# Performance work log

Hardware: AMD Instinct MI355X
Metric: run time of the kernel (lower is better)

## Reference

```python
import jax, jax.numpy as jnp
import numpy as np
import math

POOL = 7          # RoIAlign output_size
SR = 2            # sampling_ratio


def _roi_align(feat, boxes, bidx):
    """torchvision RoIAlign, aligned=False, spatial_scale=1.0, sampling_ratio=2.
    feat: [B,C,H,W]; boxes: [N,4] (x1,y1,x2,y2) in pixel coords of this level;
    bidx: [N] int batch indices. Returns [N,C,POOL,POOL]."""
    B, C, H, W = feat.shape
    x1, y1, x2, y2 = boxes[:, 0], boxes[:, 1], boxes[:, 2], boxes[:, 3]
    roi_w = jnp.maximum(x2 - x1, 1.0)
    roi_h = jnp.maximum(y2 - y1, 1.0)
    bin_w = roi_w / POOL
    bin_h = roi_h / POOL
    # sample-point offsets within the ROI, in bin units: [POOL, SR]
    off = jnp.arange(POOL, dtype=feat.dtype)[:, None] + (jnp.arange(SR, dtype=feat.dtype)[None, :] + 0.5) / SR
    ys = y1[:, None, None] + bin_h[:, None, None] * off  # [N,POOL,SR]
    xs = x1[:, None, None] + bin_w[:, None, None] * off  # [N,POOL,SR]

    def prep(c, size):
        valid = (c > -1.0) & (c < size)
        c = jnp.clip(c, 0.0, size - 1)
        lo = jnp.floor(c).astype(jnp.int32)
        hi = jnp.minimum(lo + 1, size - 1)
        return lo, hi, c - lo, valid

    y_lo, y_hi, fy, vy = prep(ys, H)
    x_lo, x_hi, fx, vx = prep(xs, W)

    b = bidx.astype(jnp.int32)[:, None, None, None, None]  # [N,1,1,1,1]

    def gather(yi, xi):
        # -> [N,POOL,SR,POOL,SR,C] (advanced indices broadcast, channel slice last)
        return feat[b, :, yi[:, :, :, None, None], xi[:, None, None, :, :]]

    hy = (1.0 - fy)[:, :, :, None, None, None]
    ly = fy[:, :, :, None, None, None]
    hx = (1.0 - fx)[:, None, None, :, :, None]
    lx = fx[:, None, None, :, :, None]
    v = (gather(y_lo, x_lo) * hy * hx + gather(y_lo, x_hi) * hy * lx
         + gather(y_hi, x_lo) * ly * hx + gather(y_hi, x_hi) * ly * lx)
    valid = (vy[:, :, :, None, None] & vx[:, None, None, :, :])[..., None]
    v = jnp.where(valid, v, 0.0)
    out = v.mean(axis=(2, 4))          # average over SRxSR samples -> [N,POOL,POOL,C]
    return out.transpose(0, 3, 1, 2)   # [N,C,POOL,POOL]


def setup_inputs() -> dict:
    key = jax.random.key(0)
    k2, k3, k4, k5, kxy, kwh, kbi = jax.random.split(key, 7)
    N = 1000
    p2 = jax.random.normal(k2, (2, 256, 256, 256), dtype=jnp.float32)
    p3 = jax.random.normal(k3, (2, 256, 128, 128), dtype=jnp.float32)
    p4 = jax.random.normal(k4, (2, 256, 64, 64), dtype=jnp.float32)
    p5 = jax.random.normal(k5, (2, 256, 32, 32), dtype=jnp.float32)
    xy = jax.random.uniform(kxy, (N, 2), minval=0.0, maxval=0.7)
    wh = jax.random.uniform(kwh, (N, 2), minval=0.02, maxval=0.3)
    rpn_bbox = jnp.concatenate([xy, xy + wh], axis=1)  # (x1,y1,x2,y2) normalized
    box_index = jax.random.randint(kbi, (N,), 0, 2, dtype=jnp.int32)
    return {"p2": p2, "p3": p3, "p4": p4, "p5": p5,
            "rpn_bbox": rpn_bbox, "box_index": box_index}


def reference(p2, p3, p4, p5, rpn_bbox, box_index):
    feats = [p2, p3, p4, p5]
    N = rpn_bbox.shape[0]
    x1, y1, x2, y2 = rpn_bbox[:, 0], rpn_bbox[:, 1], rpn_bbox[:, 2], rpn_bbox[:, 3]
    area = (y2 - y1) * (x2 - x1)
    roi_level = jnp.log(jnp.sqrt(area)) / math.log(2.0)
    roi_level = jnp.clip(jnp.round(roi_level) + 4.0, 0.0, 3.0).astype(jnp.int32)
    # Compute RoIAlign of every ROI at every level, then select per-ROI level.
    # (The masked-select / per-level dispatch / argsort-combine in the original
    # restores original ROI order, so this is mathematically identical.)
    pooled_per_level = jnp.stack(
        [_roi_align(f, rpn_bbox * f.shape[3], box_index) for f in feats], axis=0
    )  # [4, N, C, 7, 7]
    pooled = pooled_per_level[roi_level, jnp.arange(N)]  # [N, C, 7, 7]
    return pooled
```

## Files before the change

kernel.cpp:

```cpp
#include <hip/hip_runtime.h>
#include <math.h>

#define POOL 7
#define NCELL 49
#define NCH 256
#define CH_SPLIT 32
#define CHPB (NCH / CH_SPLIT)
#define CHPW (CHPB / 4)
#define LDSF 640
#define NIT_S 10
#define NBUCK 512

typedef float f32x2 __attribute__((ext_vector_type(2)));

typedef __attribute__((address_space(1))) void global_void;
typedef __attribute__((address_space(3))) void lds_void;
__device__ __forceinline__ void stage4(const float* g, float* l) {
    __builtin_amdgcn_global_load_lds((global_void*)g, (lds_void*)l, 4, 0, 0);
}
__device__ __forceinline__ void stage16(const float* g, float* l) {
    __builtin_amdgcn_global_load_lds((global_void*)g, (lds_void*)l, 16, 0, 0);
}
__device__ __forceinline__ unsigned ldsaddr(const float* p) {
    return (unsigned)(uintptr_t)(lds_void*)(void*)const_cast<float*>(p);
}

template <int V> __device__ __forceinline__ void vwait() {
    if constexpr (V == 0)       asm volatile("s_waitcnt vmcnt(0)" ::: "memory");
    else if constexpr (V == 1)  asm volatile("s_waitcnt vmcnt(1)" ::: "memory");
    else if constexpr (V == 2)  asm volatile("s_waitcnt vmcnt(2)" ::: "memory");
    else if constexpr (V == 3)  asm volatile("s_waitcnt vmcnt(3)" ::: "memory");
    else if constexpr (V == 10) asm volatile("s_waitcnt vmcnt(10)" ::: "memory");
}

struct BoxP {
    int W, bidx, y0, x0a, wwa, ngrp, x0, ww, packed;
    float x1, y1, bin_w, bin_h;
};

__device__ __forceinline__ BoxP compute_boxp(const float* boxes, const int* bidxp, int n)
{
    BoxP P;
    float bx1 = boxes[4 * n + 0], by1 = boxes[4 * n + 1];
    float bx2 = boxes[4 * n + 2], by2 = boxes[4 * n + 3];
    float area = (by2 - by1) * (bx2 - bx1);
    float lvlf = logf(sqrtf(area)) * 1.4426950408889634f;
    int level = (int)fminf(fmaxf(rintf(lvlf) + 4.0f, 0.0f), 3.0f);
    int W = 256 >> level;
    float scale = (float)W;
    P.W = W;
    P.bidx = bidxp[n];
    P.x1 = bx1 * scale;
    P.y1 = by1 * scale;
    P.bin_w = fmaxf((bx2 - bx1) * scale, 1.0f) * (1.0f / POOL);
    P.bin_h = fmaxf((by2 - by1) * scale, 1.0f) * (1.0f / POOL);

    float yA = P.y1 + P.bin_h * 0.25f, yB = P.y1 + P.bin_h * 6.75f;
    float xA = P.x1 + P.bin_w * 0.25f, xB = P.x1 + P.bin_w * 6.75f;
    int y0  = (int)floorf(fminf(fmaxf(yA, 0.f), (float)(W - 1)));
    int y1h = min((int)floorf(fminf(fmaxf(yB, 0.f), (float)(W - 1))) + 1, W - 1);
    int x0  = (int)floorf(fminf(fmaxf(xA, 0.f), (float)(W - 1)));
    x0 = min(x0, W - 2);
    int x1p = min((int)floorf(fminf(fmaxf(xB, 0.f), (float)(W - 1))) + 1, W - 1);
    int ww = x1p - x0 + 1;
    int wh = y1h - y0 + 1;

    int x0a = x0 & ~3;
    int wwa = ((x1p - x0a + 1) + 3) & ~3;
    if ((wwa & 7) == 0 && (wwa + 4) * wh <= LDSF) wwa += 4;
    int padded = wwa * wh;

    P.y0 = y0; P.x0 = x0; P.x0a = x0a; P.wwa = wwa; P.ww = ww;
    P.ngrp = (padded <= LDSF) ? (wwa >> 2) * wh : -1;
    int whc = min(wh, LDSF / ww);
    P.packed = ww * whc;
    return P;
}

struct Tab {
    int loff0[4], loff1[4];
    float w00[4], w01[4], w10[4], w11[4];
};

__device__ __forceinline__ void make_tab(Tab& tb, int lane, int W, int rs, int xb, int y0,
                                         float x1, float y1, float bin_w, float bin_h)
{
    int cell = (lane < NCELL) ? lane : (NCELL - 1);
    int py = cell / POOL, px = cell % POOL;
#pragma unroll
    for (int s = 0; s < 4; ++s) {
        int sy = s >> 1, sx = s & 1;
        float y = y1 + bin_h * ((float)py + ((float)sy + 0.5f) * 0.5f);
        float x = x1 + bin_w * ((float)px + ((float)sx + 0.5f) * 0.5f);
        bool v = (y > -1.f) && (y < (float)W) && (x > -1.f) && (x < (float)W);
        float yc = fminf(fmaxf(y, 0.f), (float)(W - 1));
        float xc = fminf(fmaxf(x, 0.f), (float)(W - 1));
        int ylo = (int)floorf(yc), xlo = (int)floorf(xc);
        int yhi = min(ylo + 1, W - 1);
        float fy = yc - (float)ylo, fx = xc - (float)xlo;
        float vv = v ? 0.25f : 0.f;
        int bxp = min(xlo, W - 2);
        bool in = (xlo == bxp);
        float wx0 = in ? (1.f - fx) : 0.f;
        float wx1 = in ? fx : 1.f;
        float wr0 = (1.f - fy) * vv, wr1 = fy * vv;
        tb.loff0[s] = (ylo - y0) * rs + (bxp - xb);
        tb.loff1[s] = (yhi - y0) * rs + (bxp - xb);
        tb.w00[s] = wr0 * wx0; tb.w01[s] = wr0 * wx1;
        tb.w10[s] = wr1 * wx0; tb.w11[s] = wr1 * wx1;
    }
}

__device__ __forceinline__ void issue_reads(const float* cb, const Tab& tb,
                                            f32x2 p0[4], f32x2 p1[4])
{
    unsigned base = ldsaddr(cb);
#pragma unroll
    for (int s = 0; s < 4; ++s) {
        unsigned a0 = base + 4u * (unsigned)tb.loff0[s];
        unsigned a1 = base + 4u * (unsigned)tb.loff1[s];
        asm volatile("ds_read2_b32 %0, %1 offset0:0 offset1:1" : "=v"(p0[s]) : "v"(a0));
        asm volatile("ds_read2_b32 %0, %1 offset0:0 offset1:1" : "=v"(p1[s]) : "v"(a1));
    }
}

__device__ __forceinline__ float finish(const Tab& tb, const f32x2 p0[4], const f32x2 p1[4])
{
    float acc = 0.f;
#pragma unroll
    for (int s = 0; s < 4; ++s) {
        acc += tb.w00[s] * p0[s].x + tb.w01[s] * p0[s].y
             + tb.w10[s] * p1[s].x + tb.w11[s] * p1[s].y;
    }
    return acc;
}

template <int NIT4>
__device__ __forceinline__ void box_x4(
    const float* fbase, float* outp, float* sm, int lane,
    int W, int HW, int wwa, int y0, int x0a, int ngrp,
    float x1, float y1, float bin_w, float bin_h)
{
    int g_off[NIT4];
    bool act[NIT4];
    int wwa4 = wwa >> 2;
#pragma unroll
    for (int k = 0; k < NIT4; ++k) {
        int idx = k * 64 + lane;
        act[k] = idx < ngrp;
        int ii = act[k] ? idx : 0;
        int r = ii / wwa4;
        int c = ii - r * wwa4;
        g_off[k] = (y0 + r) * W + x0a + c * 4;
    }
#pragma unroll
    for (int k = 0; k < NIT4; ++k)
        if (act[k]) stage16(fbase + g_off[k], sm + k * 256);
#pragma unroll
    for (int k = 0; k < NIT4; ++k)
        if (act[k]) stage16(fbase + (size_t)HW + g_off[k], sm + LDSF + k * 256);

    Tab tb;
    make_tab(tb, lane, W, wwa, x0a, y0, x1, y1, bin_w, bin_h);

    f32x2 p0[4], p1[4];
    vwait<NIT4>();
    issue_reads(sm, tb, p0, p1);
    asm volatile("s_waitcnt lgkmcnt(0)" ::: "memory");
    __builtin_amdgcn_sched_barrier(0);
    float r0 = finish(tb, p0, p1);
    if (lane < NCELL) outp[0] = r0;

    vwait<1>();
    issue_reads(sm + LDSF, tb, p0, p1);
    asm volatile("s_waitcnt lgkmcnt(0)" ::: "memory");
    __builtin_amdgcn_sched_barrier(0);
    float r1 = finish(tb, p0, p1);
    if (lane < NCELL) outp[(size_t)NCELL] = r1;
}

__device__ __forceinline__ void box_s(
    const float* fbase, float* outp, float* sm, int lane,
    int W, int HW, int ww, int y0, int x0, int packed,
    float x1, float y1, float bin_w, float bin_h)
{
    int g_off[NIT_S];
#pragma unroll
    for (int k = 0; k < NIT_S; ++k) {
        int idx = k * 64 + lane;
        idx = (idx < packed) ? idx : 0;
        int r = idx / ww;
        int c = idx - r * ww;
        g_off[k] = (y0 + r) * W + (x0 + c);
    }
#pragma unroll
    for (int k = 0; k < NIT_S; ++k) stage4(fbase + g_off[k], sm + k * 64);
#pragma unroll
    for (int k = 0; k < NIT_S; ++k) stage4(fbase + (size_t)HW + g_off[k], sm + LDSF + k * 64);

    Tab tb;
    make_tab(tb, lane, W, ww, x0, y0, x1, y1, bin_w, bin_h);

    f32x2 p0[4], p1[4];
    vwait<NIT_S>();
    issue_reads(sm, tb, p0, p1);
    asm volatile("s_waitcnt lgkmcnt(0)" ::: "memory");
    __builtin_amdgcn_sched_barrier(0);
    float r0 = finish(tb, p0, p1);
    if (lane < NCELL) outp[0] = r0;

    vwait<1>();
    issue_reads(sm + LDSF, tb, p0, p1);
    asm volatile("s_waitcnt lgkmcnt(0)" ::: "memory");
    __builtin_amdgcn_sched_barrier(0);
    float r1 = finish(tb, p0, p1);
    if (lane < NCELL) outp[(size_t)NCELL] = r1;
}

__device__ __forceinline__ int box_key(const float* boxes, const int* bidx, int n)
{
    float bx1 = boxes[4 * n + 0], by1 = boxes[4 * n + 1];
    float bx2 = boxes[4 * n + 2], by2 = boxes[4 * n + 3];
    float area = (by2 - by1) * (bx2 - bx1);
    float lvlf = logf(sqrtf(area)) * 1.4426950408889634f;
    int level = (int)fminf(fmaxf(rintf(lvlf) + 4.0f, 0.0f), 3.0f);
    int b = bidx[n] & 1;
    float cx = 0.5f * (bx1 + bx2), cy = 0.5f * (by1 + by2);
    int qx = min(7, max(0, (int)(cx * 8.0f)));
    int qy = min(7, max(0, (int)(cy * 8.0f)));
    return (((((level << 1) | b) << 3) | qy) << 3) | qx;
}

__global__ __launch_bounds__(NBUCK) void box_sort_kernel(
    const float* __restrict__ boxes, const int* __restrict__ bidx,
    int* __restrict__ perm, int* __restrict__ prm, int N)
{
    __shared__ int h0[NBUCK], h1[NBUCK];
    const int t = threadIdx.x;
    h0[t] = 0;
    __syncthreads();
    for (int n = t; n < N; n += NBUCK)
        atomicAdd(&h0[box_key(boxes, bidx, n)], 1);
    __syncthreads();
    int* src = h0; int* dst = h1;
    for (int off = 1; off < NBUCK; off <<= 1) {
        dst[t] = src[t] + ((t >= off) ? src[t - off] : 0);
        __syncthreads();
        int* tmp = src; src = dst; dst = tmp;
    }
    dst[t] = (t == 0) ? 0 : src[t - 1];
    __syncthreads();
    for (int n = t; n < N; n += NBUCK) {
        int slot = atomicAdd(&dst[box_key(boxes, bidx, n)], 1);
        perm[slot] = n;
    }
    if (prm) {
        for (int n = t; n < N; n += NBUCK) {
            BoxP P = compute_boxp(boxes, bidx, n);
            int4* o = (int4*)(prm + (size_t)n * 16);
            o[0] = make_int4(P.W, P.bidx, P.y0, P.x0a);
            o[1] = make_int4(P.wwa, P.ngrp, P.x0, P.ww);
            o[2] = make_int4(P.packed, __float_as_int(P.x1),
                             __float_as_int(P.y1), __float_as_int(P.bin_w));
            o[3] = make_int4(__float_as_int(P.bin_h), 0, 0, 0);
        }
    }
}

__global__ __launch_bounds__(256, 8) void roi_align_fpn_kernel(
    const float* __restrict__ p2, const float* __restrict__ p3,
    const float* __restrict__ p4, const float* __restrict__ p5,
    const float* __restrict__ boxes, const int* __restrict__ bidx,
    const int* __restrict__ perm, const int* __restrict__ prm,
    float* __restrict__ out, int N)
{
    __shared__ float smem[4][CHPW][LDSF];
    const int n = perm ? perm[blockIdx.y] : (int)blockIdx.y;
    const int t = threadIdx.x;
    const int wave = t >> 6;
    const int lane = t & 63;

    BoxP P;
    if (prm) {
        const int4* ip = (const int4*)(prm + (size_t)n * 16);
        int4 q0 = ip[0], q1 = ip[1], q2 = ip[2], q3 = ip[3];
        P.W = q0.x;  P.bidx = q0.y;  P.y0 = q0.z;  P.x0a = q0.w;
        P.wwa = q1.x; P.ngrp = q1.y; P.x0 = q1.z;  P.ww = q1.w;
        P.packed = q2.x;
        P.x1 = __int_as_float(q2.y); P.y1 = __int_as_float(q2.z);
        P.bin_w = __int_as_float(q2.w); P.bin_h = __int_as_float(q3.x);
    } else {
        P = compute_boxp(boxes, bidx, n);
    }
    const int W = P.W;
    const int HW = W * W;
    const float* feat = (W == 256) ? p2 : (W == 128) ? p3 : (W == 64) ? p4 : p5;
    feat += (size_t)P.bidx * NCH * HW;

    const int ch0 = blockIdx.x * CHPB + wave * CHPW;
    const float* fbase = feat + (size_t)ch0 * HW;
    float* sm = &smem[wave][0][0];
    int cell = (lane < NCELL) ? lane : (NCELL - 1);
    float* outp = out + (size_t)n * NCH * NCELL + (size_t)ch0 * NCELL + cell;

    if (P.ngrp >= 0) {
        int nit4 = (P.ngrp + 63) >> 6;
        if (nit4 == 1)      box_x4<1>(fbase, outp, sm, lane, W, HW, P.wwa, P.y0, P.x0a, P.ngrp, P.x1, P.y1, P.bin_w, P.bin_h);
        else if (nit4 == 2) box_x4<2>(fbase, outp, sm, lane, W, HW, P.wwa, P.y0, P.x0a, P.ngrp, P.x1, P.y1, P.bin_w, P.bin_h);
        else                box_x4<3>(fbase, outp, sm, lane, W, HW, P.wwa, P.y0, P.x0a, P.ngrp, P.x1, P.y1, P.bin_w, P.bin_h);
    } else {
        box_s(fbase, outp, sm, lane, W, HW, P.ww, P.y0, P.x0, P.packed, P.x1, P.y1, P.bin_w, P.bin_h);
    }
}

extern "C" void kernel_launch(void* const* d_in, const int* in_sizes, int n_in,
                              void* d_out, int out_size, void* d_ws, size_t ws_size,
                              hipStream_t stream) {
    const float* p2    = (const float*)d_in[0];
    const float* p3    = (const float*)d_in[1];
    const float* p4    = (const float*)d_in[2];
    const float* p5    = (const float*)d_in[3];
    const float* boxes = (const float*)d_in[4];
    const int*   bidx  = (const int*)d_in[5];
    float* out = (float*)d_out;
    int N = in_sizes[5];
    int* perm = nullptr;
    int* prm  = nullptr;
    size_t permB = ((size_t)N * 4 + 15) & ~(size_t)15;
    if (d_ws && ws_size >= permB + (size_t)N * 64) {
        perm = (int*)d_ws;
        prm  = (int*)((char*)d_ws + permB);
        box_sort_kernel<<<1, NBUCK, 0, stream>>>(boxes, bidx, perm, prm, N);
    } else if (d_ws && ws_size >= (size_t)N * 4) {
        perm = (int*)d_ws;
        box_sort_kernel<<<1, NBUCK, 0, stream>>>(boxes, bidx, perm, nullptr, N);
    }
    dim3 grid(CH_SPLIT, N);
    roi_align_fpn_kernel<<<grid, 256, 0, stream>>>(p2, p3, p4, p5, boxes, bidx, perm, prm, out, N);
}
```

Before: 268.7 us.

## Precompute per-box bilinear offset/weight tables in a separate kernel

Result: slower. 299.2 us (+11.3%).

```diff
diff --git a/kernel.cpp b/kernel.cpp
--- a/kernel.cpp
+++ b/kernel.cpp
@@ -10,8 +10,7 @@
 #define LDSF 640
 #define NIT_S 10
 #define NBUCK 512
-
-typedef float f32x2 __attribute__((ext_vector_type(2)));
+#define TABDW 24
 
 typedef __attribute__((address_space(1))) void global_void;
 typedef __attribute__((address_space(3))) void lds_void;
@@ -21,16 +20,8 @@
 __device__ __forceinline__ void stage16(const float* g, float* l) {
     __builtin_amdgcn_global_load_lds((global_void*)g, (lds_void*)l, 16, 0, 0);
 }
-__device__ __forceinline__ unsigned ldsaddr(const float* p) {
-    return (unsigned)(uintptr_t)(lds_void*)(void*)const_cast<float*>(p);
-}
-
-template <int V> __device__ __forceinline__ void vwait() {
-    if constexpr (V == 0)       asm volatile("s_waitcnt vmcnt(0)" ::: "memory");
-    else if constexpr (V == 1)  asm volatile("s_waitcnt vmcnt(1)" ::: "memory");
-    else if constexpr (V == 2)  asm volatile("s_waitcnt vmcnt(2)" ::: "memory");
-    else if constexpr (V == 3)  asm volatile("s_waitcnt vmcnt(3)" ::: "memory");
-    else if constexpr (V == 10) asm volatile("s_waitcnt vmcnt(10)" ::: "memory");
+__device__ __forceinline__ void vwait0() {
+    asm volatile("s_waitcnt vmcnt(0)" ::: "memory");
 }
 
 struct BoxP {
@@ -77,13 +68,14 @@
     return P;
 }
 
-struct Tab {
-    int loff0[4], loff1[4];
+struct TabR {
+    int o0[4], o1[4];
     float w00[4], w01[4], w10[4], w11[4];
 };
 
-__device__ __forceinline__ void make_tab(Tab& tb, int lane, int W, int rs, int xb, int y0,
-                                         float x1, float y1, float bin_w, float bin_h)
+__device__ __forceinline__ void make_tab_arrays(
+    int lane, int W, int rs, int xb, int y0,
+    float x1, float y1, float bin_w, float bin_h, TabR& tb)
 {
     int cell = (lane < NCELL) ? lane : (NCELL - 1);
     int py = cell / POOL, px = cell % POOL;
@@ -104,33 +96,23 @@
         float wx0 = in ? (1.f - fx) : 0.f;
         float wx1 = in ? fx : 1.f;
         float wr0 = (1.f - fy) * vv, wr1 = fy * vv;
-        tb.loff0[s] = (ylo - y0) * rs + (bxp - xb);
-        tb.loff1[s] = (yhi - y0) * rs + (bxp - xb);
+        tb.o0[s] = ((ylo - y0) * rs + (bxp - xb)) * 4;
+        tb.o1[s] = ((yhi - y0) * rs + (bxp - xb)) * 4;
         tb.w00[s] = wr0 * wx0; tb.w01[s] = wr0 * wx1;
         tb.w10[s] = wr1 * wx0; tb.w11[s] = wr1 * wx1;
     }
 }
 
-__device__ __forceinline__ void issue_reads(const float* cb, const Tab& tb,
-                                            f32x2 p0[4], f32x2 p1[4])
-{
-    unsigned base = ldsaddr(cb);
+__device__ __forceinline__ float consume(const float* cb, const TabR& tb)
+{
+    const char* b = (const char*)cb;
+    float acc = 0.f;
 #pragma unroll
     for (int s = 0; s < 4; ++s) {
-        unsigned a0 = base + 4u * (unsigned)tb.loff0[s];
-        unsigned a1 = base + 4u * (unsigned)tb.loff1[s];
-        asm volatile("ds_read2_b32 %0, %1 offset0:0 offset1:1" : "=v"(p0[s]) : "v"(a0));
-        asm volatile("ds_read2_b32 %0, %1 offset0:0 offset1:1" : "=v"(p1[s]) : "v"(a1));
-    }
-}
-
-__device__ __forceinline__ float finish(const Tab& tb, const f32x2 p0[4], const f32x2 p1[4])
-{
-    float acc = 0.f;
-#pragma unroll
-    for (int s = 0; s < 4; ++s) {
-        acc += tb.w00[s] * p0[s].x + tb.w01[s] * p0[s].y
-             + tb.w10[s] * p1[s].x + tb.w11[s] * p1[s].y;
+        const float* q0 = (const float*)(b + tb.o0[s]);
+        const float* q1 = (const float*)(b + tb.o1[s]);
+        acc += tb.w00[s] * q0[0] + tb.w01[s] * q0[1]
+             + tb.w10[s] * q1[0] + tb.w11[s] * q1[1];
     }
     return acc;
 }
@@ -138,8 +120,7 @@
 template <int NIT4>
 __device__ __forceinline__ void box_x4(
     const float* fbase, float* outp, float* sm, int lane,
-    int W, int HW, int wwa, int y0, int x0a, int ngrp,
-    float x1, float y1, float bin_w, float bin_h)
+    int W, int HW, int wwa, int y0, int x0a, int ngrp, const TabR& tb)
 {
     int g_off[NIT4];
     bool act[NIT4];
@@ -160,29 +141,16 @@
     for (int k = 0; k < NIT4; ++k)
         if (act[k]) stage16(fbase + (size_t)HW + g_off[k], sm + LDSF + k * 256);
 
-    Tab tb;
-    make_tab(tb, lane, W, wwa, x0a, y0, x1, y1, bin_w, bin_h);
-
-    f32x2 p0[4], p1[4];
-    vwait<NIT4>();
-    issue_reads(sm, tb, p0, p1);
-    asm volatile("s_waitcnt lgkmcnt(0)" ::: "memory");
-    __builtin_amdgcn_sched_barrier(0);
-    float r0 = finish(tb, p0, p1);
+    vwait0();
+    float r0 = consume(sm, tb);
     if (lane < NCELL) outp[0] = r0;
-
-    vwait<1>();
-    issue_reads(sm + LDSF, tb, p0, p1);
-    asm volatile("s_waitcnt lgkmcnt(0)" ::: "memory");
-    __builtin_amdgcn_sched_barrier(0);
-    float r1 = finish(tb, p0, p1);
+    float r1 = consume(sm + LDSF, tb);
     if (lane < NCELL) outp[(size_t)NCELL] = r1;
 }
 
 __device__ __forceinline__ void box_s(
     const float* fbase, float* outp, float* sm, int lane,
-    int W, int HW, int ww, int y0, int x0, int packed,
-    float x1, float y1, float bin_w, float bin_h)
+    int W, int HW, int ww, int y0, int x0, int packed, const TabR& tb)
 {
     int g_off[NIT_S];
 #pragma unroll
@@ -198,22 +166,10 @@
 #pragma unroll
     for (int k = 0; k < NIT_S; ++k) stage4(fbase + (size_t)HW + g_off[k], sm + LDSF + k * 64);
 
-    Tab tb;
-    make_tab(tb, lane, W, ww, x0, y0, x1, y1, bin_w, bin_h);
-
-    f32x2 p0[4], p1[4];
-    vwait<NIT_S>();
-    issue_reads(sm, tb, p0, p1);
-    asm volatile("s_waitcnt lgkmcnt(0)" ::: "memory");
-    __builtin_amdgcn_sched_barrier(0);
-    float r0 = finish(tb, p0, p1);
+    vwait0();
+    float r0 = consume(sm, tb);
     if (lane < NCELL) outp[0] = r0;
-
-    vwait<1>();
-    issue_reads(sm + LDSF, tb, p0, p1);
-    asm volatile("s_waitcnt lgkmcnt(0)" ::: "memory");
-    __builtin_amdgcn_sched_barrier(0);
-    float r1 = finish(tb, p0, p1);
+    float r1 = consume(sm + LDSF, tb);
     if (lane < NCELL) outp[(size_t)NCELL] = r1;
 }
 
@@ -267,11 +223,37 @@
     }
 }
 
+__global__ __launch_bounds__(256) void box_tab_kernel(
+    const float* __restrict__ boxes, const int* __restrict__ bidx,
+    int* __restrict__ tab, int N)
+{
+    int wid = blockIdx.x * 4 + (threadIdx.x >> 6);
+    int lane = threadIdx.x & 63;
+    if (wid >= N) return;
+    BoxP P = compute_boxp(boxes, bidx, wid);
+    int rs = (P.ngrp >= 0) ? P.wwa : P.ww;
+    int xb = (P.ngrp >= 0) ? P.x0a : P.x0;
+    TabR tb;
+    make_tab_arrays(lane, P.W, rs, xb, P.y0, P.x1, P.y1, P.bin_w, P.bin_h, tb);
+    int4* d = (int4*)(tab + ((size_t)wid * 64 + lane) * TABDW);
+    d[0] = make_int4(tb.o0[0], tb.o0[1], tb.o0[2], tb.o0[3]);
+    d[1] = make_int4(tb.o1[0], tb.o1[1], tb.o1[2], tb.o1[3]);
+    d[2] = make_int4(__float_as_int(tb.w00[0]), __float_as_int(tb.w01[0]),
+                     __float_as_int(tb.w00[1]), __float_as_int(tb.w01[1]));
+    d[3] = make_int4(__float_as_int(tb.w00[2]), __float_as_int(tb.w01[2]),
+                     __float_as_int(tb.w00[3]), __float_as_int(tb.w01[3]));
+    d[4] = make_int4(__float_as_int(tb.w10[0]), __float_as_int(tb.w11[0]),
+                     __float_as_int(tb.w10[1]), __float_as_int(tb.w11[1]));
+    d[5] = make_int4(__float_as_int(tb.w10[2]), __float_as_int(tb.w11[2]),
+                     __float_as_int(tb.w10[3]), __float_as_int(tb.w11[3]));
+}
+
 __global__ __launch_bounds__(256, 8) void roi_align_fpn_kernel(
     const float* __restrict__ p2, const float* __restrict__ p3,
     const float* __restrict__ p4, const float* __restrict__ p5,
     const float* __restrict__ boxes, const int* __restrict__ bidx,
     const int* __restrict__ perm, const int* __restrict__ prm,
+    const int* __restrict__ tab,
     float* __restrict__ out, int N)
 {
     __shared__ float smem[4][CHPW][LDSF];
@@ -292,6 +274,27 @@
     } else {
         P = compute_boxp(boxes, bidx, n);
     }
+
+    TabR tb;
+    if (tab) {
+        const int4* tp = (const int4*)(tab + ((size_t)n * 64 + lane) * TABDW);
+        int4 a = tp[0], b = tp[1], c = tp[2], d = tp[3], e = tp[4], f = tp[5];
+        tb.o0[0] = a.x; tb.o0[1] = a.y; tb.o0[2] = a.z; tb.o0[3] = a.w;
+        tb.o1[0] = b.x; tb.o1[1] = b.y; tb.o1[2] = b.z; tb.o1[3] = b.w;
+        tb.w00[0] = __int_as_float(c.x); tb.w01[0] = __int_as_float(c.y);
+        tb.w00[1] = __int_as_float(c.z); tb.w01[1] = __int_as_float(c.w);
+        tb.w00[2] = __int_as_float(d.x); tb.w01[2] = __int_as_float(d.y);
+        tb.w00[3] = __int_as_float(d.z); tb.w01[3] = __int_as_float(d.w);
+        tb.w10[0] = __int_as_float(e.x); tb.w11[0] = __int_as_float(e.y);
+        tb.w10[1] = __int_as_float(e.z); tb.w11[1] = __int_as_float(e.w);
+        tb.w10[2] = __int_as_float(f.x); tb.w11[2] = __int_as_float(f.y);
+        tb.w10[3] = __int_as_float(f.z); tb.w11[3] = __int_as_float(f.w);
+    } else {
+        int rs = (P.ngrp >= 0) ? P.wwa : P.ww;
+        int xb = (P.ngrp >= 0) ? P.x0a : P.x0;
+        make_tab_arrays(lane, P.W, rs, xb, P.y0, P.x1, P.y1, P.bin_w, P.bin_h, tb);
+    }
+
     const int W = P.W;
     const int HW = W * W;
     const float* feat = (W == 256) ? p2 : (W == 128) ? p3 : (W == 64) ? p4 : p5;
@@ -305,11 +308,11 @@
 
     if (P.ngrp >= 0) {
         int nit4 = (P.ngrp + 63) >> 6;
-        if (nit4 == 1)      box_x4<1>(fbase, outp, sm, lane, W, HW, P.wwa, P.y0, P.x0a, P.ngrp, P.x1, P.y1, P.bin_w, P.bin_h);
-        else if (nit4 == 2) box_x4<2>(fbase, outp, sm, lane, W, HW, P.wwa, P.y0, P.x0a, P.ngrp, P.x1, P.y1, P.bin_w, P.bin_h);
-        else                box_x4<3>(fbase, outp, sm, lane, W, HW, P.wwa, P.y0, P.x0a, P.ngrp, P.x1, P.y1, P.bin_w, P.bin_h);
+        if (nit4 == 1)      box_x4<1>(fbase, outp, sm, lane, W, HW, P.wwa, P.y0, P.x0a, P.ngrp, tb);
+        else if (nit4 == 2) box_x4<2>(fbase, outp, sm, lane, W, HW, P.wwa, P.y0, P.x0a, P.ngrp, tb);
+        else                box_x4<3>(fbase, outp, sm, lane, W, HW, P.wwa, P.y0, P.x0a, P.ngrp, tb);
     } else {
-        box_s(fbase, outp, sm, lane, W, HW, P.ww, P.y0, P.x0, P.packed, P.x1, P.y1, P.bin_w, P.bin_h);
+        box_s(fbase, outp, sm, lane, W, HW, P.ww, P.y0, P.x0, P.packed, tb);
     }
 }
 
@@ -326,8 +329,17 @@
     int N = in_sizes[5];
     int* perm = nullptr;
     int* prm  = nullptr;
+    int* tab  = nullptr;
     size_t permB = ((size_t)N * 4 + 15) & ~(size_t)15;
-    if (d_ws && ws_size >= permB + (size_t)N * 64) {
+    size_t prmB  = (size_t)N * 64;
+    size_t tabB  = (size_t)N * 64 * TABDW * 4;
+    if (d_ws && ws_size >= permB + prmB + tabB) {
+        perm = (int*)d_ws;
+        prm  = (int*)((char*)d_ws + permB);
+        tab  = (int*)((char*)d_ws + permB + prmB);
+        box_sort_kernel<<<1, NBUCK, 0, stream>>>(boxes, bidx, perm, prm, N);
+        box_tab_kernel<<<(N + 3) / 4, 256, 0, stream>>>(boxes, bidx, tab, N);
+    } else if (d_ws && ws_size >= permB + prmB) {
         perm = (int*)d_ws;
         prm  = (int*)((char*)d_ws + permB);
         box_sort_kernel<<<1, NBUCK, 0, stream>>>(boxes, bidx, perm, prm, N);
@@ -336,5 +348,5 @@
         box_sort_kernel<<<1, NBUCK, 0, stream>>>(boxes, bidx, perm, nullptr, N);
     }
     dim3 grid(CH_SPLIT, N);
-    roi_align_fpn_kernel<<<grid, 256, 0, stream>>>(p2, p3, p4, p5, boxes, bidx, perm, prm, out, N);
-}
+    roi_align_fpn_kernel<<<grid, 256, 0, stream>>>(p2, p3, p4, p5, boxes, bidx, perm, prm, tab, out, N);
+}
```
